# Kernel tuning notes

Hardware: AMD Instinct MI355X
Metric: run time of the kernel (lower is better)

The kernel has to match this reference:

```python
import jax, jax.numpy as jnp
import numpy as np

B, S, D = 4, 2048, 1024
H = 16
HD = D // H

def setup_inputs() -> dict:
    key = jax.random.key(0)
    ks = jax.random.split(key, 6)
    scale = 1.0 / np.sqrt(D)
    x = jax.random.normal(ks[0], (B, S, D), dtype=jnp.float32)
    Wq = jax.random.normal(ks[1], (D, D), dtype=jnp.float32) * scale
    Wk = jax.random.normal(ks[2], (D, D), dtype=jnp.float32) * scale
    Wv = jax.random.normal(ks[3], (D, D), dtype=jnp.float32) * scale
    Wo = jax.random.normal(ks[4], (D, D), dtype=jnp.float32) * scale
    bo = jax.random.normal(ks[5], (D,), dtype=jnp.float32) * 0.01
    return {"x": x, "Wq": Wq, "Wk": Wk, "Wv": Wv, "Wo": Wo, "bo": bo}

def reference(x, Wq, Wk, Wv, Wo, bo):
    b, n, _ = x.shape
    # QKV projections (no bias), split into heads: [b, h, n, hd]
    q = (x @ Wq).reshape(b, n, H, HD).transpose(0, 2, 1, 3)
    k = (x @ Wk).reshape(b, n, H, HD).transpose(0, 2, 1, 3)
    v = (x @ Wv).reshape(b, n, H, HD).transpose(0, 2, 1, 3)
    scores = jnp.einsum('bhqd,bhkd->bhqk', q, k) / jnp.sqrt(jnp.float32(HD))
    causal = jnp.tril(jnp.ones((n, n), dtype=bool))
    scores = jnp.where(causal, scores, -jnp.inf)
    attn = jax.nn.softmax(scores, axis=-1)  # dropout p=0.0 -> identity
    ctx = jnp.einsum('bhqk,bhkd->bhqd', attn, v)
    ctx = ctx.transpose(0, 2, 1, 3).reshape(b, n, D)
    return ctx @ Wo + bo
```

## Files before the change

### kernel.cpp

```cpp
#include <hip/hip_runtime.h>

#define S_   2048
#define D_   1024
#define H_   16
#define HD_  64
#define NTOK 8192
#define QKS  2048
#define QSCALE 0.18033688f

typedef __attribute__((ext_vector_type(8))) __bf16 bf16x8;
typedef __attribute__((ext_vector_type(4))) __bf16 bf16x4;
typedef __attribute__((ext_vector_type(4))) float  f32x4;
typedef __attribute__((ext_vector_type(4))) short  short4v;

#define GPTR(p) ((__attribute__((address_space(1))) void*)(unsigned long long)(p))
#define LPTR(p) ((__attribute__((address_space(3))) void*)(p))

__global__ __launch_bounds__(256) void k_prep(const float* __restrict__ x,
                                              __bf16* __restrict__ xb,
                                              const float* __restrict__ Wq,
                                              const float* __restrict__ Wk,
                                              const float* __restrict__ Wv,
                                              const float* __restrict__ Wo,
                                              __bf16* __restrict__ wqkt,
                                              __bf16* __restrict__ wvt,
                                              __bf16* __restrict__ wot) {
    const int bx = blockIdx.x;
    if (bx < 4096) {
        int i = bx * 2048 + threadIdx.x * 8;
        f32x4 a = *(const f32x4*)(x + i);
        f32x4 b = *(const f32x4*)(x + i + 4);
        bf16x8 o;
#pragma unroll
        for (int j = 0; j < 4; j++) { o[j] = (__bf16)a[j]; o[4 + j] = (__bf16)b[j]; }
        *(bf16x8*)(xb + i) = o;
        return;
    }
    __shared__ float t[32][33];
    const int tt = bx - 4096;
    const int widx = tt >> 10, r = tt & 1023;
    const float* W;
    __bf16* Wt;
    switch (widx) {
        case 0: W = Wq; Wt = wqkt; break;
        case 1: W = Wk; Wt = wqkt + (size_t)D_ * D_; break;
        case 2: W = Wv; Wt = wvt; break;
        default: W = Wo; Wt = wot; break;
    }
    const int i0 = (r & 31) * 32, j0 = (r >> 5) * 32;
    const int tx = threadIdx.x & 31, ty = threadIdx.x >> 5;
#pragma unroll
    for (int rr = 0; rr < 32; rr += 8)
        t[ty + rr][tx] = W[(size_t)(i0 + ty + rr) * D_ + j0 + tx];
    __syncthreads();
#pragma unroll
    for (int rr = 0; rr < 32; rr += 8)
        Wt[(size_t)(j0 + ty + rr) * D_ + i0 + tx] = (__bf16)t[tx][ty + rr];
}

__device__ __forceinline__ void gemm_body_bf16(const __bf16* __restrict__ A,
                                               const __bf16* __restrict__ Bt,
                                               __bf16* __restrict__ C,
                                               int N, int K, int tm, int tn,
                                               float scale, int vperm,
                                               __bf16* As, __bf16* Bs) {
    const int tid  = threadIdx.x;
    const int wave = tid >> 6, lane = tid & 63;
    const int quad = lane >> 4, l16 = lane & 15;
    const int wm = (wave & 1) * 64, wn = (wave >> 1) * 64;
    f32x4 acc[4][4] = {};

    for (int k0 = 0; k0 < K; k0 += 32) {
        __syncthreads();
#pragma unroll
        for (int s = 0; s < 2; s++) {
            const int cb = s * 256 + wave * 64;
            const int c  = cb + lane;
            const int row = c >> 2;
            const int kc  = ((c & 3) ^ ((row >> 1) & 3)) * 8;
            __builtin_amdgcn_global_load_lds(GPTR(A + (size_t)(tm + row) * K + k0 + kc),
                                             LPTR(As + cb * 8), 16, 0, 0);
            __builtin_amdgcn_global_load_lds(GPTR(Bt + (size_t)(tn + row) * K + k0 + kc),
                                             LPTR(Bs + cb * 8), 16, 0, 0);
        }
        __syncthreads();

        bf16x8 af[4], bf[4];
#pragma unroll
        for (int mi = 0; mi < 4; mi++) {
            const int rf = wm + mi * 16 + l16;
            af[mi] = *(const bf16x8*)&As[rf * 32 + (quad ^ ((rf >> 1) & 3)) * 8];
        }
#pragma unroll
        for (int ni = 0; ni < 4; ni++) {
            const int rf = wn + ni * 16 + l16;
            bf[ni] = *(const bf16x8*)&Bs[rf * 32 + (quad ^ ((rf >> 1) & 3)) * 8];
        }
#pragma unroll
        for (int mi = 0; mi < 4; mi++)
#pragma unroll
            for (int ni = 0; ni < 4; ni++)
                acc[mi][ni] = __builtin_amdgcn_mfma_f32_16x16x32_bf16(
                    af[mi], bf[ni], acc[mi][ni], 0, 0, 0);
    }

#pragma unroll
    for (int mi = 0; mi < 4; mi++)
#pragma unroll
        for (int ni = 0; ni < 4; ni++)
#pragma unroll
            for (int r = 0; r < 4; r++) {
                const int row = tm + wm + mi * 16 + quad * 4 + r;
                const int col = tn + wn + ni * 16 + l16;
                const int xr  = (vperm & (row >> 3) & 1) << 2;
                C[(size_t)row * N + (col ^ xr)] = (__bf16)(acc[mi][ni][r] * scale);
            }
}

__global__ __launch_bounds__(256) void k_gemm_qkv(const __bf16* __restrict__ xb,
                                                  const __bf16* __restrict__ wqkt,
                                                  const __bf16* __restrict__ wvt,
                                                  __bf16* __restrict__ qk,
                                                  __bf16* __restrict__ VT) {
    __shared__ __bf16 As[128 * 32];
    __shared__ __bf16 Bs[128 * 32];
    const int bx = blockIdx.x;
    if (bx < 1024) {
        const int tm = (bx & 63) * 128, tn = (bx >> 6) * 128;
        const float scale = (tn < D_) ? QSCALE : 1.0f;
        gemm_body_bf16(xb, wqkt, qk, QKS, D_, tm, tn, scale, 0, As, Bs);
    } else {
        const int b2 = bx - 1024;
        const int tn = (b2 & 63) * 128, tm = (b2 >> 6) * 128;
        gemm_body_bf16(wvt, xb, VT, NTOK, D_, tm, tn, 1.0f, 1, As, Bs);
    }
}

__global__ __launch_bounds__(256) void k_gemm_o(const __bf16* __restrict__ A,
                                                const __bf16* __restrict__ Bt,
                                                float* __restrict__ C,
                                                const float* __restrict__ bias) {
    __shared__ __bf16 As[128 * 32];
    __shared__ __bf16 Bs[128 * 32];
    const int tid  = threadIdx.x;
    const int wave = tid >> 6, lane = tid & 63;
    const int quad = lane >> 4, l16 = lane & 15;
    const int tm = blockIdx.x * 128, tn = blockIdx.y * 128;
    const int wm = (wave & 1) * 64, wn = (wave >> 1) * 64;
    const int N = D_, K = D_;
    f32x4 acc[4][4] = {};

    for (int k0 = 0; k0 < K; k0 += 32) {
        __syncthreads();
#pragma unroll
        for (int s = 0; s < 2; s++) {
            const int cb = s * 256 + wave * 64;
            const int c  = cb + lane;
            const int row = c >> 2;
            const int kc  = ((c & 3) ^ ((row >> 1) & 3)) * 8;
            __builtin_amdgcn_global_load_lds(GPTR(A + (size_t)(tm + row) * K + k0 + kc),
                                             LPTR(As + cb * 8), 16, 0, 0);
            __builtin_amdgcn_global_load_lds(GPTR(Bt + (size_t)(tn + row) * K + k0 + kc),
                                             LPTR(Bs + cb * 8), 16, 0, 0);
        }
        __syncthreads();

        bf16x8 af[4], bf[4];
#pragma unroll
        for (int mi = 0; mi < 4; mi++) {
            const int rf = wm + mi * 16 + l16;
            af[mi] = *(const bf16x8*)&As[rf * 32 + (quad ^ ((rf >> 1) & 3)) * 8];
        }
#pragma unroll
        for (int ni = 0; ni < 4; ni++) {
            const int rf = wn + ni * 16 + l16;
            bf[ni] = *(const bf16x8*)&Bs[rf * 32 + (quad ^ ((rf >> 1) & 3)) * 8];
        }
#pragma unroll
        for (int mi = 0; mi < 4; mi++)
#pragma unroll
            for (int ni = 0; ni < 4; ni++)
                acc[mi][ni] = __builtin_amdgcn_mfma_f32_16x16x32_bf16(
                    af[mi], bf[ni], acc[mi][ni], 0, 0, 0);
    }

#pragma unroll
    for (int mi = 0; mi < 4; mi++)
#pragma unroll
        for (int ni = 0; ni < 4; ni++)
#pragma unroll
            for (int r = 0; r < 4; r++) {
                const int row = tm + wm + mi * 16 + quad * 4 + r;
                const int col = tn + wn + ni * 16 + l16;
                C[(size_t)row * N + col] = acc[mi][ni][r] + bias[col];
            }
}

__device__ __forceinline__ short bf16_bits(float f) {
    __bf16 h = (__bf16)f;
    return __builtin_bit_cast(short, h);
}

__global__ __launch_bounds__(256, 4) void k_attn(const __bf16* __restrict__ Qb,
                                                 const __bf16* __restrict__ Kb,
                                                 const __bf16* __restrict__ VT,
                                                 __bf16* __restrict__ ctx) {
    __shared__ __bf16 Ks[2][64 * 64];
    __shared__ __bf16 Vs[2][64 * 64];

    const int tid = threadIdx.x;
    const int wave = tid >> 6, lane = tid & 63;
    const int quad = lane >> 4, l16 = lane & 15;
    const int bid = blockIdx.x;
    const int hb  = ((bid >> 7) << 3) | (bid & 7);
    const int qp  = (bid >> 3) & 15;
    const int h = hb >> 2, b = hb & 3;
    const size_t tok0 = (size_t)b * S_;
    const size_t hoff = (size_t)h * HD_;

    auto stage = [&](int kv, int buf) {
#pragma unroll
        for (int s = 0; s < 2; s++) {
            const int cb = s * 256 + wave * 64;
            const int c  = cb + lane;
            const int row = c >> 3;
            const int gc  = (c & 7) ^ (row & 7);
            __builtin_amdgcn_global_load_lds(
                GPTR(Kb + (size_t)(tok0 + kv + row) * QKS + hoff + gc * 8),
                LPTR(&Ks[buf][cb * 8]), 16, 0, 0);
            __builtin_amdgcn_global_load_lds(
                GPTR(VT + (hoff + row) * (size_t)NTOK + tok0 + kv + gc * 8),
                LPTR(&Vs[buf][cb * 8]), 16, 0, 0);
        }
    };

#pragma unroll 1
    for (int pass = 0; pass < 2; pass++) {
        const int j  = pass == 0 ? 31 - qp : qp;
        const int qb = j * 64;
        const int q0 = qb + wave * 16;

        bf16x8 qf[2];
#pragma unroll
        for (int ks = 0; ks < 2; ks++)
            qf[ks] = *(const bf16x8*)&Qb[(tok0 + q0 + l16) * QKS +
                                         hoff + ks * 32 + quad * 8];

        f32x4 oacc[4] = {};
        float lsum = 0.f;
        const int ktb = j;

        stage(0, 0);
        __syncthreads();

        for (int kt = 0; kt <= ktb; kt++) {
            const int cur = kt & 1;
            const int kv0 = kt * 64;
            if (kt < ktb) stage(kv0 + 64, 1 - cur);

            if (kv0 <= q0 + 15) {
                f32x4 st[4] = {};
#pragma unroll
                for (int ks = 0; ks < 2; ks++)
#pragma unroll
                    for (int ksub = 0; ksub < 4; ksub++) {
                        const int r = ksub * 16 + l16;
                        bf16x8 kf = *(const bf16x8*)
                            &Ks[cur][(r * 8 + (((ks * 4 + quad) ^ (r & 7)))) * 8];
                        st[ksub] = __builtin_amdgcn_mfma_f32_16x16x32_bf16(
                            kf, qf[ks], st[ksub], 0, 0, 0);
                    }
                if (kv0 + 63 > q0) {
#pragma unroll
                    for (int ksub = 0; ksub < 4; ksub++)
#pragma unroll
                        for (int r = 0; r < 4; r++) {
                            const int kg = kv0 + ksub * 16 + quad * 4 + r;
                            const int qg = q0 + l16;
                            if (kg > qg) st[ksub][r] = -1e30f;
                        }
                }
                short4v pfrag[4];
#pragma unroll
                for (int ksub = 0; ksub < 4; ksub++) {
                    float p0 = __builtin_amdgcn_exp2f(st[ksub][0]);
                    float p1 = __builtin_amdgcn_exp2f(st[ksub][1]);
                    float p2 = __builtin_amdgcn_exp2f(st[ksub][2]);
                    float p3 = __builtin_amdgcn_exp2f(st[ksub][3]);
                    lsum += (p0 + p1) + (p2 + p3);
                    short4v pf = {bf16_bits(p0), bf16_bits(p1),
                                  bf16_bits(p2), bf16_bits(p3)};
                    pfrag[ksub] = pf;
                }
#pragma unroll
                for (int ksub = 0; ksub < 4; ksub++)
#pragma unroll
                    for (int hs = 0; hs < 4; hs++) {
                        const int row = hs * 16 + l16;
                        const int swz = (ksub * 2 + (quad >> 1)) ^ (row & 7);
                        short4v vf = *(const short4v*)
                            &Vs[cur][row * 64 + swz * 8 + ((quad ^ (l16 >> 3)) & 1) * 4];
                        oacc[hs] = __builtin_amdgcn_mfma_f32_16x16x16bf16_1k(
                            vf, pfrag[ksub], oacc[hs], 0, 0, 0);
                    }
            }
            __syncthreads();
        }

        {
            float v = lsum;
            v += __shfl_xor(v, 16);
            v += __shfl_xor(v, 32);
            const float rl = 1.0f / v;
#pragma unroll
            for (int hs = 0; hs < 4; hs++) {
                bf16x4 o;
#pragma unroll
                for (int r = 0; r < 4; r++) o[r] = (__bf16)(oacc[hs][r] * rl);
                *(bf16x4*)&ctx[(tok0 + q0 + l16) * D_ + hoff +
                               hs * 16 + quad * 4] = o;
            }
        }
    }
}

extern "C" void kernel_launch(void* const* d_in, const int* in_sizes, int n_in,
                              void* d_out, int out_size, void* d_ws, size_t ws_size,
                              hipStream_t stream) {
    const float* x  = (const float*)d_in[0];
    const float* Wq = (const float*)d_in[1];
    const float* Wk = (const float*)d_in[2];
    const float* Wv = (const float*)d_in[3];
    const float* Wo = (const float*)d_in[4];
    const float* bo = (const float*)d_in[5];
    float* out = (float*)d_out;

    char* p = (char*)d_ws;
    __bf16* xb   = (__bf16*)p; p += (size_t)NTOK * D_ * 2;
    __bf16* wqkt = (__bf16*)p; p += (size_t)2 * D_ * D_ * 2;
    __bf16* wvt  = (__bf16*)p; p += (size_t)D_ * D_ * 2;
    __bf16* wot  = (__bf16*)p; p += (size_t)D_ * D_ * 2;
    __bf16* qk   = (__bf16*)p; p += (size_t)NTOK * QKS * 2;
    __bf16* VT   = (__bf16*)p; p += (size_t)NTOK * D_ * 2;
    __bf16* ctx  = xb;

    k_prep<<<dim3(4096 + 4 * 1024), 256, 0, stream>>>(x, xb, Wq, Wk, Wv, Wo,
                                                      wqkt, wvt, wot);
    k_gemm_qkv<<<dim3(1024 + 512), 256, 0, stream>>>(xb, wqkt, wvt, qk, VT);
    k_attn<<<dim3(1024), 256, 0, stream>>>(qk, qk + D_, VT, ctx);
    k_gemm_o<<<dim3(64, 8), 256, 0, stream>>>(ctx, wot, out, bo);
}
```

Baseline: 234.8 us.

## Merge four kernels into two cooperative launches with grid-wide syncs

Fuses prep with the QKV GEMM, and attention with the output projection, into two cooperative kernels separated by grid.sync(), so two kernel launches and their boundaries go away. Occupancy is checked at runtime, and the code falls back to the original four-kernel path if 6 or 4 blocks per CU are not resident. The cost is that each fused kernel waits on its slowest block at the barrier, with only 512 of 1024 blocks doing the output GEMM. The fused kernels also need enough blocks resident at once, and the launch bounds are tighter (256,6) for the prep+QKV kernel.

Result: slower. 242.4 us (+3.2%).

```diff
diff --git a/kernel.cpp b/kernel.cpp
--- a/kernel.cpp
+++ b/kernel.cpp
@@ -1,4 +1,7 @@
 #include <hip/hip_runtime.h>
+#include <hip/hip_cooperative_groups.h>
+
+namespace cg = cooperative_groups;
 
 #define S_   2048
 #define D_   1024
@@ -16,18 +19,18 @@
 #define GPTR(p) ((__attribute__((address_space(1))) void*)(unsigned long long)(p))
 #define LPTR(p) ((__attribute__((address_space(3))) void*)(p))
 
-__global__ __launch_bounds__(256) void k_prep(const float* __restrict__ x,
-                                              __bf16* __restrict__ xb,
-                                              const float* __restrict__ Wq,
-                                              const float* __restrict__ Wk,
-                                              const float* __restrict__ Wv,
-                                              const float* __restrict__ Wo,
-                                              __bf16* __restrict__ wqkt,
-                                              __bf16* __restrict__ wvt,
-                                              __bf16* __restrict__ wot) {
-    const int bx = blockIdx.x;
-    if (bx < 4096) {
-        int i = bx * 2048 + threadIdx.x * 8;
+__device__ __forceinline__ void prep_unit(int u, const float* __restrict__ x,
+                                          __bf16* __restrict__ xb,
+                                          const float* __restrict__ Wq,
+                                          const float* __restrict__ Wk,
+                                          const float* __restrict__ Wv,
+                                          const float* __restrict__ Wo,
+                                          __bf16* __restrict__ wqkt,
+                                          __bf16* __restrict__ wvt,
+                                          __bf16* __restrict__ wot,
+                                          float* __restrict__ ts) {
+    if (u < 4096) {
+        int i = u * 2048 + threadIdx.x * 8;
         f32x4 a = *(const f32x4*)(x + i);
         f32x4 b = *(const f32x4*)(x + i + 4);
         bf16x8 o;
@@ -36,8 +39,8 @@
         *(bf16x8*)(xb + i) = o;
         return;
     }
-    __shared__ float t[32][33];
-    const int tt = bx - 4096;
+    float (*t)[33] = (float(*)[33])ts;
+    const int tt = u - 4096;
     const int widx = tt >> 10, r = tt & 1023;
     const float* W;
     __bf16* Wt;
@@ -56,6 +59,7 @@
 #pragma unroll
     for (int rr = 0; rr < 32; rr += 8)
         Wt[(size_t)(j0 + ty + rr) * D_ + i0 + tx] = (__bf16)t[tx][ty + rr];
+    __syncthreads();
 }
 
 __device__ __forceinline__ void gemm_body_bf16(const __bf16* __restrict__ A,
@@ -117,14 +121,10 @@
             }
 }
 
-__global__ __launch_bounds__(256) void k_gemm_qkv(const __bf16* __restrict__ xb,
-                                                  const __bf16* __restrict__ wqkt,
-                                                  const __bf16* __restrict__ wvt,
-                                                  __bf16* __restrict__ qk,
-                                                  __bf16* __restrict__ VT) {
-    __shared__ __bf16 As[128 * 32];
-    __shared__ __bf16 Bs[128 * 32];
-    const int bx = blockIdx.x;
+__device__ __forceinline__ void qkv_block(int bx, const __bf16* xb,
+                                          const __bf16* wqkt, const __bf16* wvt,
+                                          __bf16* qk, __bf16* VT,
+                                          __bf16* As, __bf16* Bs) {
     if (bx < 1024) {
         const int tm = (bx & 63) * 128, tn = (bx >> 6) * 128;
         const float scale = (tn < D_) ? QSCALE : 1.0f;
@@ -136,16 +136,15 @@
     }
 }
 
-__global__ __launch_bounds__(256) void k_gemm_o(const __bf16* __restrict__ A,
-                                                const __bf16* __restrict__ Bt,
-                                                float* __restrict__ C,
-                                                const float* __restrict__ bias) {
-    __shared__ __bf16 As[128 * 32];
-    __shared__ __bf16 Bs[128 * 32];
+__device__ __forceinline__ void gemmo_body(int bid, const __bf16* __restrict__ A,
+                                           const __bf16* __restrict__ Bt,
+                                           float* __restrict__ C,
+                                           const float* __restrict__ bias,
+                                           __bf16* As, __bf16* Bs) {
     const int tid  = threadIdx.x;
     const int wave = tid >> 6, lane = tid & 63;
     const int quad = lane >> 4, l16 = lane & 15;
-    const int tm = blockIdx.x * 128, tn = blockIdx.y * 128;
+    const int tm = (bid & 63) * 128, tn = (bid >> 6) * 128;
     const int wm = (wave & 1) * 64, wn = (wave >> 1) * 64;
     const int N = D_, K = D_;
     f32x4 acc[4][4] = {};
@@ -201,17 +200,15 @@
     return __builtin_bit_cast(short, h);
 }
 
-__global__ __launch_bounds__(256, 4) void k_attn(const __bf16* __restrict__ Qb,
-                                                 const __bf16* __restrict__ Kb,
-                                                 const __bf16* __restrict__ VT,
-                                                 __bf16* __restrict__ ctx) {
-    __shared__ __bf16 Ks[2][64 * 64];
-    __shared__ __bf16 Vs[2][64 * 64];
-
+__device__ __forceinline__ void attn_body(int bid, const __bf16* __restrict__ Qb,
+                                          const __bf16* __restrict__ Kb,
+                                          const __bf16* __restrict__ VT,
+                                          __bf16* __restrict__ ctx,
+                                          __bf16 (*Ks)[64 * 64],
+                                          __bf16 (*Vs)[64 * 64]) {
     const int tid = threadIdx.x;
     const int wave = tid >> 6, lane = tid & 63;
     const int quad = lane >> 4, l16 = lane & 15;
-    const int bid = blockIdx.x;
     const int hb  = ((bid >> 7) << 3) | (bid & 7);
     const int qp  = (bid >> 3) & 15;
     const int h = hb >> 2, b = hb & 3;
@@ -324,6 +321,86 @@
     }
 }
 
+
+__global__ __launch_bounds__(256, 6) void k_prep_qkv(const float* __restrict__ x,
+                                                     __bf16* __restrict__ xb,
+                                                     const float* __restrict__ Wq,
+                                                     const float* __restrict__ Wk,
+                                                     const float* __restrict__ Wv,
+                                                     const float* __restrict__ Wo,
+                                                     __bf16* __restrict__ wqkt,
+                                                     __bf16* __restrict__ wvt,
+                                                     __bf16* __restrict__ wot,
+                                                     __bf16* __restrict__ qk,
+                                                     __bf16* __restrict__ VT) {
+    __shared__ __bf16 As[128 * 32];
+    __shared__ __bf16 Bs[128 * 32];
+    const int bid = blockIdx.x;
+    for (int u = bid; u < 8192; u += 1536)
+        prep_unit(u, x, xb, Wq, Wk, Wv, Wo, wqkt, wvt, wot, (float*)As);
+    __threadfence();
+    cg::this_grid().sync();
+    qkv_block(bid, xb, wqkt, wvt, qk, VT, As, Bs);
+}
+
+__global__ __launch_bounds__(256, 4) void k_attn_o(const __bf16* __restrict__ Qb,
+                                                   const __bf16* __restrict__ Kb,
+                                                   const __bf16* __restrict__ VT,
+                                                   __bf16* __restrict__ ctx,
+                                                   const __bf16* __restrict__ wot,
+                                                   float* __restrict__ out,
+                                                   const float* __restrict__ bias) {
+    __shared__ __bf16 Ks[2][64 * 64];
+    __shared__ __bf16 Vs[2][64 * 64];
+    const int bid = blockIdx.x;
+    attn_body(bid, Qb, Kb, VT, ctx, Ks, Vs);
+    __threadfence();
+    cg::this_grid().sync();
+    if (bid < 512)
+        gemmo_body(bid, ctx, wot, out, bias, (__bf16*)Ks, (__bf16*)Vs);
+}
+
+__global__ __launch_bounds__(256) void k_prep(const float* __restrict__ x,
+                                              __bf16* __restrict__ xb,
+                                              const float* __restrict__ Wq,
+                                              const float* __restrict__ Wk,
+                                              const float* __restrict__ Wv,
+                                              const float* __restrict__ Wo,
+                                              __bf16* __restrict__ wqkt,
+                                              __bf16* __restrict__ wvt,
+                                              __bf16* __restrict__ wot) {
+    __shared__ float t[32][33];
+    prep_unit(blockIdx.x, x, xb, Wq, Wk, Wv, Wo, wqkt, wvt, wot, (float*)t);
+}
+
+__global__ __launch_bounds__(256) void k_gemm_qkv(const __bf16* __restrict__ xb,
+                                                  const __bf16* __restrict__ wqkt,
+                                                  const __bf16* __restrict__ wvt,
+                                                  __bf16* __restrict__ qk,
+                                                  __bf16* __restrict__ VT) {
+    __shared__ __bf16 As[128 * 32];
+    __shared__ __bf16 Bs[128 * 32];
+    qkv_block(blockIdx.x, xb, wqkt, wvt, qk, VT, As, Bs);
+}
+
+__global__ __launch_bounds__(256, 4) void k_attn(const __bf16* __restrict__ Qb,
+                                                 const __bf16* __restrict__ Kb,
+                                                 const __bf16* __restrict__ VT,
+                                                 __bf16* __restrict__ ctx) {
+    __shared__ __bf16 Ks[2][64 * 64];
+    __shared__ __bf16 Vs[2][64 * 64];
+    attn_body(blockIdx.x, Qb, Kb, VT, ctx, Ks, Vs);
+}
+
+__global__ __launch_bounds__(256) void k_gemm_o(const __bf16* __restrict__ A,
+                                                const __bf16* __restrict__ Bt,
+                                                float* __restrict__ C,
+                                                const float* __restrict__ bias) {
+    __shared__ __bf16 As[128 * 32];
+    __shared__ __bf16 Bs[128 * 32];
+    gemmo_body(blockIdx.x + blockIdx.y * 64, A, Bt, C, bias, As, Bs);
+}
+
 extern "C" void kernel_launch(void* const* d_in, const int* in_sizes, int n_in,
                               void* d_out, int out_size, void* d_ws, size_t ws_size,
                               hipStream_t stream) {
@@ -343,10 +420,31 @@
     __bf16* qk   = (__bf16*)p; p += (size_t)NTOK * QKS * 2;
     __bf16* VT   = (__bf16*)p; p += (size_t)NTOK * D_ * 2;
     __bf16* ctx  = xb;
-
-    k_prep<<<dim3(4096 + 4 * 1024), 256, 0, stream>>>(x, xb, Wq, Wk, Wv, Wo,
-                                                      wqkt, wvt, wot);
-    k_gemm_qkv<<<dim3(1024 + 512), 256, 0, stream>>>(xb, wqkt, wvt, qk, VT);
-    k_attn<<<dim3(1024), 256, 0, stream>>>(qk, qk + D_, VT, ctx);
-    k_gemm_o<<<dim3(64, 8), 256, 0, stream>>>(ctx, wot, out, bo);
-}
+    __bf16* Kb   = qk + D_;
+
+    static int mode = -1;
+    if (mode < 0) {
+        int b1 = 0, b2 = 0;
+        hipOccupancyMaxActiveBlocksPerMultiprocessor(&b1, k_prep_qkv, 256, 0);
+        hipOccupancyMaxActiveBlocksPerMultiprocessor(&b2, k_attn_o, 256, 0);
+        mode = (b1 >= 6 && b2 >= 4) ? 1 : 0;
+    }
+
+    if (mode == 1) {
+        void* a1[] = {(void*)&x, (void*)&xb, (void*)&Wq, (void*)&Wk, (void*)&Wv,
+                      (void*)&Wo, (void*)&wqkt, (void*)&wvt, (void*)&wot,
+                      (void*)&qk, (void*)&VT};
+        hipLaunchCooperativeKernel((const void*)k_prep_qkv, dim3(1536), dim3(256),
+                                   a1, 0, stream);
+        void* a2[] = {(void*)&qk, (void*)&Kb, (void*)&VT, (void*)&ctx,
+                      (void*)&wot, (void*)&out, (void*)&bo};
+        hipLaunchCooperativeKernel((const void*)k_attn_o, dim3(1024), dim3(256),
+                                   a2, 0, stream);
+    } else {
+        k_prep<<<dim3(8192), 256, 0, stream>>>(x, xb, Wq, Wk, Wv, Wo,
+                                               wqkt, wvt, wot);
+        k_gemm_qkv<<<dim3(1024 + 512), 256, 0, stream>>>(xb, wqkt, wvt, qk, VT);
+        k_attn<<<dim3(1024), 256, 0, stream>>>(qk, Kb, VT, ctx);
+        k_gemm_o<<<dim3(64, 8), 256, 0, stream>>>(ctx, wot, out, bo);
+    }
+}
```
